# Performance work log

Hardware: AMD Instinct MI355X
Metric: run time of the kernel (lower is better)

Reference implementation:

```python
import jax, jax.numpy as jnp
import numpy as np

B, S, HID = 2, 2048, 2048
H, DH = 16, 128
SCALE = 1.0 / np.sqrt(DH)


def setup_inputs() -> dict:
    key = jax.random.key(0)
    ks = jax.random.split(key, 5)
    std = 1.0 / np.sqrt(HID)
    return {
        "x": jax.random.normal(ks[0], (B, S, HID), dtype=jnp.float32),
        "wq": jax.random.normal(ks[1], (HID, HID), dtype=jnp.float32) * std,
        "wk": jax.random.normal(ks[2], (HID, HID), dtype=jnp.float32) * std,
        "wv": jax.random.normal(ks[3], (HID, HID), dtype=jnp.float32) * std,
        "wo": jax.random.normal(ks[4], (HID, HID), dtype=jnp.float32) * std,
    }


def reference(x, wq, wk, wv, wo):
    # nn.Linear(h, h, bias=False): y = x @ W^T
    q = (x @ wq.T).reshape(B, S, H, DH).transpose(0, 2, 1, 3)  # [B,H,S,Dh]
    k = (x @ wk.T).reshape(B, S, H, DH).transpose(0, 2, 1, 3)
    v = (x @ wv.T).reshape(B, S, H, DH).transpose(0, 2, 1, 3)
    scores = jnp.einsum("bhsd,bhtd->bhst", q, k) * SCALE  # [B,H,S,S]
    attn = jax.nn.softmax(scores.astype(jnp.float32), axis=-1).astype(q.dtype)
    # dropout p=0.0 (eval): identity
    out = jnp.einsum("bhst,bhtd->bhsd", attn, v)  # [B,H,S,Dh]
    out = out.transpose(0, 2, 1, 3).reshape(B, S, HID)
    return out @ wo.T
```

## Files before the change

### kernel.cpp

```cpp
#include <hip/hip_runtime.h>
#include <hip/hip_bf16.h>
#include <stdint.h>

typedef __attribute__((ext_vector_type(8))) short short8;
typedef __attribute__((ext_vector_type(4))) float f32x4;
typedef __attribute__((ext_vector_type(4))) unsigned int uint4v;

static __device__ __forceinline__ ushort f2bf(float f) {
    uint32_t u = __builtin_bit_cast(uint32_t, f);
    uint32_t r = (u + 0x7FFFu + ((u >> 16) & 1u)) >> 16;
    return (ushort)r;
}

static __device__ __forceinline__ uint32_t cvt_pk_bf16(float lo, float hi) {
    uint32_t d;
    asm("v_cvt_pk_bf16_f32 %0, %1, %2" : "=v"(d) : "v"(lo), "v"(hi));
    return d;
}

static __device__ __forceinline__ void async_copy16(const void* g, void* l) {
    __builtin_amdgcn_global_load_lds(
        (const __attribute__((address_space(1))) uint32_t*)g,
        (__attribute__((address_space(3))) uint32_t*)l, 16, 0, 0);
}

__global__ __launch_bounds__(256) void cast_kernel(const float* __restrict__ in,
                                                   ushort* __restrict__ out, int n4) {
    int i = blockIdx.x * 256 + threadIdx.x;
    if (i >= n4) return;
    float4 v = reinterpret_cast<const float4*>(in)[i];
    uint2 o;
    o.x = cvt_pk_bf16(v.x, v.y);
    o.y = cvt_pk_bf16(v.z, v.w);
    reinterpret_cast<uint2*>(out)[i] = o;
}

__global__ __launch_bounds__(256) void cast3_kernel(const float* __restrict__ a,
                                                    const float* __restrict__ b,
                                                    const float* __restrict__ c,
                                                    ushort* __restrict__ out, int n4each) {
    int i = blockIdx.x * 256 + threadIdx.x;
    int which = i / n4each;
    int j = i - which * n4each;
    const float* src = which == 0 ? a : (which == 1 ? b : c);
    if (which > 2) return;
    float4 v = reinterpret_cast<const float4*>(src)[j];
    uint2 o;
    o.x = cvt_pk_bf16(v.x, v.y);
    o.y = cvt_pk_bf16(v.z, v.w);
    reinterpret_cast<uint2*>(out)[i] = o;
}

static __device__ __forceinline__ void store_val(float* C, size_t idx, float v) { C[idx] = v; }
static __device__ __forceinline__ void store_val(ushort* C, size_t idx, float v) { C[idx] = f2bf(v); }

template <typename OutT>
__global__ __launch_bounds__(256) void gemm_bt_kernel(const ushort* __restrict__ A,
                                                      const ushort* __restrict__ B,
                                                      OutT* __restrict__ C,
                                                      int M, int N, int K) {
    __shared__ __align__(16) ushort As[128 * 32];
    __shared__ __align__(16) ushort Bs[128 * 32];
    const int tid = threadIdx.x;
    const int w = tid >> 6, lane = tid & 63;
    const int fr = lane & 15, fq = lane >> 4;
    const int wr = w >> 1, wc = w & 1;
    const int bpn = N >> 7;
    const int which = blockIdx.x / bpn;
    const int row0 = blockIdx.y * 128;
    const int gcol0 = blockIdx.x * 128;
    const int col0 = gcol0 - which * N;
    OutT* Cw = C + (size_t)which * M * N;

    const int srow = tid >> 2;
    const int scol = (tid & 3) * 8;
    const ushort* ga0 = A + (size_t)(row0 + srow) * K + scol;
    const ushort* ga1 = A + (size_t)(row0 + 64 + srow) * K + scol;
    const ushort* gb0 = B + (size_t)(gcol0 + srow) * K + scol;
    const ushort* gb1 = B + (size_t)(gcol0 + 64 + srow) * K + scol;
    ushort* la0 = &As[(w * 64) * 8];
    ushort* la1 = &As[(256 + w * 64) * 8];
    ushort* lb0 = &Bs[(w * 64) * 8];
    ushort* lb1 = &Bs[(256 + w * 64) * 8];

    f32x4 acc[4][4];
#pragma unroll
    for (int m = 0; m < 4; ++m)
#pragma unroll
        for (int n = 0; n < 4; ++n) acc[m][n] = f32x4{0.f, 0.f, 0.f, 0.f};

    for (int kt = 0; kt < K; kt += 32) {
        __syncthreads();
        async_copy16(ga0 + kt, la0);
        async_copy16(ga1 + kt, la1);
        async_copy16(gb0 + kt, lb0);
        async_copy16(gb1 + kt, lb1);
        __syncthreads();
        short8 af[4], bfr[4];
#pragma unroll
        for (int m = 0; m < 4; ++m)
            af[m] = *(const short8*)&As[(wr * 64 + m * 16 + fr) * 32 + fq * 8];
#pragma unroll
        for (int n = 0; n < 4; ++n)
            bfr[n] = *(const short8*)&Bs[(wc * 64 + n * 16 + fr) * 32 + fq * 8];
#pragma unroll
        for (int m = 0; m < 4; ++m)
#pragma unroll
            for (int n = 0; n < 4; ++n)
                acc[m][n] = __builtin_amdgcn_mfma_f32_16x16x32_bf16(af[m], bfr[n], acc[m][n], 0, 0, 0);
    }

#pragma unroll
    for (int m = 0; m < 4; ++m) {
        const int grow = row0 + wr * 64 + m * 16 + fq * 4;
#pragma unroll
        for (int n = 0; n < 4; ++n) {
            const int gcol = col0 + wc * 64 + n * 16 + fr;
#pragma unroll
            for (int r = 0; r < 4; ++r)
                store_val(Cw, (size_t)(grow + r) * N + gcol, acc[m][n][r]);
        }
    }
}

__global__ __launch_bounds__(512, 2) void gemm256_kernel(const ushort* __restrict__ A,
                                                         const ushort* __restrict__ B,
                                                         ushort* __restrict__ C,
                                                         int M, int N, int K) {
    __shared__ __align__(16) char smem[131072];
    const int tid = threadIdx.x, w = tid >> 6, lane = tid & 63;
    const int fr = lane & 15, fq = lane >> 4;
    const int wm = w >> 2, wn = w & 3;
    const int bpn = N >> 8;
    const int which = blockIdx.x / bpn;
    const int row0 = blockIdx.y * 256;
    const int gcol0 = blockIdx.x * 256;
    const int col0 = gcol0 - which * N;
    ushort* Cw = C + (size_t)which * M * N;

    const int lo = ((tid & 7) ^ ((tid >> 3) & 7)) << 4;
    const int r0p = ((tid >> 3) << 1) + (lo >> 6);
    const int colE = (lo & 63) >> 1;
    const ushort* Ap0 = A + (size_t)(row0 + r0p) * K + colE;
    const ushort* Ap1 = A + (size_t)(row0 + 128 + r0p) * K + colE;
    const ushort* Bp0 = B + (size_t)(gcol0 + r0p) * K + colE;
    const ushort* Bp1 = B + (size_t)(gcol0 + 128 + r0p) * K + colE;

    char* aregs = smem;
    char* bregs = smem + 65536;
    const int wbyte = w * 1024;

    auto stageH = [&](int h) {
        const int kc = (h >> 1) * 64 + (h & 1) * 32;
        char* ar = aregs + (h & 3) * 16384;
        char* br = bregs + (h & 3) * 16384;
        async_copy16(Ap0 + kc, ar + wbyte);
        async_copy16(Ap1 + kc, ar + 8192 + wbyte);
        async_copy16(Bp0 + kc, br + wbyte);
        async_copy16(Bp1 + kc, br + 8192 + wbyte);
    };

    const int swz = ((fr & 1) * 64 + fq * 16) ^ (((fr >> 1) & 7) << 4);
    const int aBase = (wm * 64 + (fr >> 1)) * 128 + swz;
    const int bBase = (wn * 32 + (fr >> 1)) * 128 + swz;

    f32x4 acc[8][4];
#pragma unroll
    for (int m = 0; m < 8; ++m)
#pragma unroll
        for (int n = 0; n < 4; ++n) acc[m][n] = f32x4{0.f, 0.f, 0.f, 0.f};

    const int nH = K >> 5;
    stageH(0); stageH(1); stageH(2);
    asm volatile("s_waitcnt vmcnt(8)\n\ts_barrier" ::: "memory");

    for (int i = 0; i < nH; ++i) {
        if (i + 3 < nH) stageH(i + 3);
        const char* ar = aregs + (i & 3) * 16384 + aBase;
        const char* br = bregs + (i & 3) * 16384 + bBase;
        short8 af[8], bf[4];
#pragma unroll
        for (int m = 0; m < 8; ++m) af[m] = *(const short8*)(ar + m * 1024);
#pragma unroll
        for (int n = 0; n < 4; ++n) bf[n] = *(const short8*)(br + n * 1024);
        __builtin_amdgcn_s_setprio(1);
#pragma unroll
        for (int m = 0; m < 8; ++m)
#pragma unroll
            for (int n = 0; n < 4; ++n)
                acc[m][n] = __builtin_amdgcn_mfma_f32_16x16x32_bf16(af[m], bf[n], acc[m][n], 0, 0, 0);
        __builtin_amdgcn_s_setprio(0);
        if (i < nH - 3)
            asm volatile("s_waitcnt vmcnt(8)\n\ts_barrier" ::: "memory");
        else if (i == nH - 3)
            asm volatile("s_waitcnt vmcnt(4)\n\ts_barrier" ::: "memory");
        else if (i == nH - 2)
            asm volatile("s_waitcnt vmcnt(0)\n\ts_barrier" ::: "memory");
    }

#pragma unroll
    for (int m = 0; m < 8; ++m) {
        const int grow = row0 + wm * 128 + m * 16 + fq * 4;
#pragma unroll
        for (int n = 0; n < 4; ++n) {
            const int gcol = col0 + wn * 64 + n * 16 + fr;
#pragma unroll
            for (int r2 = 0; r2 < 4; ++r2)
                Cw[(size_t)(grow + r2) * N + gcol] = f2bf(acc[m][n][r2]);
        }
    }
}

__global__ __launch_bounds__(512) void attn_kernel(const ushort* __restrict__ Q,
                                                   const ushort* __restrict__ K,
                                                   const ushort* __restrict__ VT,
                                                   ushort* __restrict__ O,
                                                   int S, int HID, float scale) {
    __shared__ __align__(16) ushort Ks[64 * 128];
    __shared__ __align__(16) ushort Vts[128 * 64];

    const int tid = threadIdx.x, w = tid >> 6, lane = tid & 63;
    const int fr = lane & 15, fq = lane >> 4;
    const int h = blockIdx.x & 15, b = blockIdx.x >> 4, qt = blockIdx.y;
    const size_t rs = (size_t)HID;
    const size_t vs = (size_t)(2 * S);
    const int qr0 = qt * 128 + w * 16;
    const float c1 = scale * 1.4426950408889634f;

    short8 qf[4];
    {
        const ushort* qp = Q + ((size_t)(b * S) + qr0 + fr) * rs + h * 128 + fq * 8;
#pragma unroll
        for (int ks = 0; ks < 4; ++ks) qf[ks] = *(const short8*)(qp + ks * 32);
    }

    f32x4 of[8];
#pragma unroll
    for (int n = 0; n < 8; ++n) of[n] = f32x4{0.f, 0.f, 0.f, 0.f};
    float m2 = -1e30f;
    float l = 0.f;

    const ushort* Kb = K + (size_t)(b * S) * rs + h * 128;
    const ushort* Vb = VT + (size_t)(h * 128) * vs + b * S;

    size_t koff[2];
#pragma unroll
    for (int j = 0; j < 2; ++j) {
        int row = j * 32 + w * 4 + (lane >> 4);
        int colb = ((lane & 15) * 16) ^ ((row & 7) << 4);
        koff[j] = (size_t)row * rs + (colb >> 1);
    }
    size_t vtoff[2];
#pragma unroll
    for (int j = 0; j < 2; ++j) {
        int row = j * 64 + (tid >> 3);
        int colb = ((tid & 7) * 16) ^ ((row & 7) << 4);
        vtoff[j] = (size_t)row * vs + (colb >> 1);
    }

    const int srcA = fr + 16 * ((2 * fq) & 3);
    const int srcB = fr + 16 * ((2 * fq + 1) & 3);
    const int par = fq >> 1;

    const int nt = S / 64;
    for (int t = 0; t < nt; ++t) {
        __syncthreads();
        const ushort* kt0 = Kb + (size_t)t * 64 * rs;
        const ushort* vt0 = Vb + (size_t)t * 64;
#pragma unroll
        for (int j = 0; j < 2; ++j)
            async_copy16(kt0 + koff[j], &Ks[j * 4096 + w * 512]);
#pragma unroll
        for (int j = 0; j < 2; ++j)
            async_copy16(vt0 + vtoff[j], &Vts[j * 4096 + w * 512]);
        __syncthreads();

        f32x4 sf[4];
        __builtin_amdgcn_s_setprio(1);
#pragma unroll
        for (int kc = 0; kc < 4; ++kc) {
            f32x4 s = f32x4{0.f, 0.f, 0.f, 0.f};
#pragma unroll
            for (int ks = 0; ks < 4; ++ks) {
                int row = kc * 16 + fr;
                int pb = (row * 256 + ks * 64 + fq * 16) ^ ((row & 7) << 4);
                short8 kf = *(const short8*)((const char*)Ks + pb);
                s = __builtin_amdgcn_mfma_f32_16x16x32_bf16(kf, qf[ks], s, 0, 0, 0);
            }
            sf[kc] = s;
        }
        __builtin_amdgcn_s_setprio(0);

        float pm = fmaxf(fmaxf(fmaxf(sf[0][0], sf[0][1]), fmaxf(sf[0][2], sf[0][3])),
                         fmaxf(fmaxf(sf[1][0], sf[1][1]), fmaxf(sf[1][2], sf[1][3])));
        pm = fmaxf(pm, fmaxf(fmaxf(fmaxf(sf[2][0], sf[2][1]), fmaxf(sf[2][2], sf[2][3])),
                             fmaxf(fmaxf(sf[3][0], sf[3][1]), fmaxf(sf[3][2], sf[3][3]))));
        pm = fmaxf(pm, __shfl_xor(pm, 16));
        pm = fmaxf(pm, __shfl_xor(pm, 32));
        float pm2 = pm * c1;
        const bool noresc = __all(pm2 - m2 <= 8.0f);
        float sc = 1.0f;
        if (!noresc) {
            float m2new = fmaxf(m2, pm2);
            sc = exp2f(m2 - m2new);
            m2 = m2new;
        }
        float rsum = 0.f;
#pragma unroll
        for (int kc = 0; kc < 4; ++kc)
#pragma unroll
            for (int r = 0; r < 4; ++r) {
                float p = exp2f(sf[kc][r] * c1 - m2);
                sf[kc][r] = p;
                rsum += p;
            }
        rsum += __shfl_xor(rsum, 16);
        rsum += __shfl_xor(rsum, 32);
        if (noresc) {
            l = l + rsum;
        } else {
            l = l * sc + rsum;
#pragma unroll
            for (int n = 0; n < 8; ++n) {
                f32x4 o = of[n];
                o[0] *= sc; o[1] *= sc; o[2] *= sc; o[3] *= sc;
                of[n] = o;
            }
        }

        uint32_t cpk[4][2];
#pragma unroll
        for (int kc = 0; kc < 4; ++kc)
#pragma unroll
            for (int hh = 0; hh < 2; ++hh)
                cpk[kc][hh] = cvt_pk_bf16(sf[kc][2 * hh], sf[kc][2 * hh + 1]);

        __builtin_amdgcn_s_setprio(1);
#pragma unroll
        for (int kvc = 0; kvc < 2; ++kvc) {
            uint32_t eA0 = __shfl(cpk[2 * kvc][0], srcA), eA1 = __shfl(cpk[2 * kvc][1], srcA);
            uint32_t oA0 = __shfl(cpk[2 * kvc + 1][0], srcA), oA1 = __shfl(cpk[2 * kvc + 1][1], srcA);
            uint32_t eB0 = __shfl(cpk[2 * kvc][0], srcB), eB1 = __shfl(cpk[2 * kvc][1], srcB);
            uint32_t oB0 = __shfl(cpk[2 * kvc + 1][0], srcB), oB1 = __shfl(cpk[2 * kvc + 1][1], srcB);
            uint4v pd;
            pd[0] = par ? oA0 : eA0; pd[1] = par ? oA1 : eA1;
            pd[2] = par ? oB0 : eB0; pd[3] = par ? oB1 : eB1;
            short8 pf = __builtin_bit_cast(short8, pd);
#pragma unroll
            for (int n = 0; n < 8; ++n) {
                int row = n * 16 + fr;
                int pb = row * 128 + ((kvc * 64 + fq * 16) ^ ((row & 7) << 4));
                short8 vf = *(const short8*)((const char*)Vts + pb);
                of[n] = __builtin_amdgcn_mfma_f32_16x16x32_bf16(vf, pf, of[n], 0, 0, 0);
            }
        }
        __builtin_amdgcn_s_setprio(0);
    }

    float inv = 1.f / l;
    ushort* ob = O + ((size_t)(b * S) + qr0 + fr) * rs + h * 128 + fq * 4;
#pragma unroll
    for (int n = 0; n < 8; ++n) {
        uint2 o2;
        o2.x = cvt_pk_bf16(of[n][0] * inv, of[n][1] * inv);
        o2.y = cvt_pk_bf16(of[n][2] * inv, of[n][3] * inv);
        *reinterpret_cast<uint2*>(ob + n * 16) = o2;
    }
}

extern "C" void kernel_launch(void* const* d_in, const int* in_sizes, int n_in,
                              void* d_out, int out_size, void* d_ws, size_t ws_size,
                              hipStream_t stream) {
    constexpr int B = 2, S = 2048, HID = 2048, H = 16;
    constexpr int M = B * S;
    const float scale = 0.08838834764831845f;

    const float* x  = (const float*)d_in[0];
    const float* wq = (const float*)d_in[1];
    const float* wk = (const float*)d_in[2];
    const float* wv = (const float*)d_in[3];
    const float* wo = (const float*)d_in[4];
    float* out = (float*)d_out;

    char* ws = (char*)d_ws;
    ushort* xb  = (ushort*)(ws);
    ushort* wqb = (ushort*)(ws + 16777216);
    ushort* wvb = (ushort*)(ws + 33554432);
    ushort* qb  = (ushort*)(ws + 41943040);
    ushort* kb  = (ushort*)(ws + 58720256);
    ushort* vtb = (ushort*)(ws + 75497472);

    const int XN = M * HID;
    const int WN = HID * HID;

    cast_kernel<<<XN / 4 / 256, 256, 0, stream>>>(x, xb, XN / 4);
    cast3_kernel<<<3 * WN / 4 / 256, 256, 0, stream>>>(wq, wk, wv, wqb, WN / 4);

    dim3 gq(2 * HID / 256, M / 256);
    gemm256_kernel<<<gq, 512, 0, stream>>>(xb, wqb, qb, M, HID, HID);

    dim3 gv(M / 128, HID / 128);
    gemm_bt_kernel<ushort><<<gv, 256, 0, stream>>>(wvb, xb, vtb, HID, M, HID);

    dim3 ga(H * B, S / 128);
    attn_kernel<<<ga, 512, 0, stream>>>(qb, kb, vtb, xb, S, HID, scale);

    cast_kernel<<<WN / 4 / 256, 256, 0, stream>>>(wo, wqb, WN / 4);
    dim3 gg(HID / 128, M / 128);
    gemm_bt_kernel<float><<<gg, 256, 0, stream>>>(xb, wqb, out, M, HID, HID);
}
```

Measured before the change: 322.7 us.

## Double-buffer K/V tiles in attention with async prefetch of next tile

Attention kernel now keeps two LDS buffers for the K and V^T tiles and issues async global-to-LDS copies for tile t+1 before computing on tile t. Explicit vmcnt waits and barriers replace the two full __syncthreads, so load latency should overlap with MFMA work. LDS use doubles (64KB), which may reduce occupancy. The hand-written waitcnt counts must match the outstanding loads exactly.

```diff
diff --git a/kernel.cpp b/kernel.cpp
--- a/kernel.cpp
+++ b/kernel.cpp
@@ -216,8 +216,8 @@
                                                    const ushort* __restrict__ VT,
                                                    ushort* __restrict__ O,
                                                    int S, int HID, float scale) {
-    __shared__ __align__(16) ushort Ks[64 * 128];
-    __shared__ __align__(16) ushort Vts[128 * 64];
+    __shared__ __align__(16) ushort Ks[2][64 * 128];
+    __shared__ __align__(16) ushort Vts[2][128 * 64];
 
     const int tid = threadIdx.x, w = tid >> 6, lane = tid & 63;
     const int fr = lane & 15, fq = lane >> 4;
@@ -258,22 +258,38 @@
         vtoff[j] = (size_t)row * vs + (colb >> 1);
     }
 
+    auto stage = [&](int t) {
+        const int bufb = t & 1;
+        const ushort* kt0 = Kb + (size_t)t * 64 * rs;
+        const ushort* vt0 = Vb + (size_t)t * 64;
+#pragma unroll
+        for (int j = 0; j < 2; ++j)
+            async_copy16(kt0 + koff[j], &Ks[bufb][j * 4096 + w * 512]);
+#pragma unroll
+        for (int j = 0; j < 2; ++j)
+            async_copy16(vt0 + vtoff[j], &Vts[bufb][j * 4096 + w * 512]);
+    };
+
     const int srcA = fr + 16 * ((2 * fq) & 3);
     const int srcB = fr + 16 * ((2 * fq + 1) & 3);
     const int par = fq >> 1;
 
     const int nt = S / 64;
+    stage(0);
     for (int t = 0; t < nt; ++t) {
-        __syncthreads();
-        const ushort* kt0 = Kb + (size_t)t * 64 * rs;
-        const ushort* vt0 = Vb + (size_t)t * 64;
-#pragma unroll
-        for (int j = 0; j < 2; ++j)
-            async_copy16(kt0 + koff[j], &Ks[j * 4096 + w * 512]);
-#pragma unroll
-        for (int j = 0; j < 2; ++j)
-            async_copy16(vt0 + vtoff[j], &Vts[j * 4096 + w * 512]);
-        __syncthreads();
+        __builtin_amdgcn_s_barrier();
+        __builtin_amdgcn_sched_barrier(0);
+        if (t + 1 < nt) {
+            stage(t + 1);
+            asm volatile("s_waitcnt vmcnt(4)" ::: "memory");
+        } else {
+            asm volatile("s_waitcnt vmcnt(0)" ::: "memory");
+        }
+        __builtin_amdgcn_s_barrier();
+        __builtin_amdgcn_sched_barrier(0);
+
+        const char* kbase = (const char*)&Ks[t & 1][0];
+        const char* vbase = (const char*)&Vts[t & 1][0];
 
         f32x4 sf[4];
         __builtin_amdgcn_s_setprio(1);
@@ -284,7 +300,7 @@
             for (int ks = 0; ks < 4; ++ks) {
                 int row = kc * 16 + fr;
                 int pb = (row * 256 + ks * 64 + fq * 16) ^ ((row & 7) << 4);
-                short8 kf = *(const short8*)((const char*)Ks + pb);
+                short8 kf = *(const short8*)(kbase + pb);
                 s = __builtin_amdgcn_mfma_f32_16x16x32_bf16(kf, qf[ks], s, 0, 0, 0);
             }
             sf[kc] = s;
@@ -350,7 +366,7 @@
             for (int n = 0; n < 8; ++n) {
                 int row = n * 16 + fr;
                 int pb = row * 128 + ((kvc * 64 + fq * 16) ^ ((row & 7) << 4));
-                short8 vf = *(const short8*)((const char*)Vts + pb);
+                short8 vf = *(const short8*)(vbase + pb);
                 of[n] = __builtin_amdgcn_mfma_f32_16x16x32_bf16(vf, pf, of[n], 0, 0, 0);
             }
         }
```

Measured after the change: 323.1 us. About the same (+0.1%).
